# Optimization experiments

Measured on AMD Instinct MI355X. Metric: run time of the kernel, lower is better.

## Reference

```python
import jax, jax.numpy as jnp
import numpy as np

THRESH = 0.5
MARGIN = 0.1
SCALE_POS = 2.0
SCALE_NEG = 40.0
EPSILON = 1e-5


def setup_inputs() -> dict:
    key = jax.random.key(0)
    k1, k2, k3 = jax.random.split(key, 3)
    B, D = 8192, 1024
    feats = jax.random.normal(k1, (B, D), dtype=jnp.float32)
    labels = jax.random.randint(k2, (B,), 0, 128, dtype=jnp.int64)
    score = jax.random.normal(k3, (B, 3), dtype=jnp.float32)
    return {"feats": feats, "labels": labels, "score": score, "type_idx": 1}


def reference(feats, labels, score, type_idx):
    B = feats.shape[0]
    # L2 normalize (torch F.normalize eps=1e-12)
    norm = jnp.maximum(jnp.linalg.norm(feats, axis=1, keepdims=True), 1e-12)
    f = feats / norm
    sim = f @ f.T  # [B, B]

    tmp = jnp.argmax(score, axis=-1) == type_idx          # [B] selected samples
    eq = labels[:, None] == labels[None, :]               # same-label
    pair = tmp[:, None] & tmp[None, :]                    # both selected

    mask_pos_all = pair & eq                              # includes diagonal, like torch mask[i]
    count = jnp.sum(mask_pos_all, axis=1)                 # torch: sum(mask[i])
    pos0 = mask_pos_all & (sim < 1.0 - EPSILON)           # pos_pair_ after <1-eps filter
    neg0 = pair & (~eq)                                   # neg_pair_

    min_pos = jnp.min(jnp.where(pos0, sim, jnp.inf), axis=1)   # min(pos_pair_)
    max_neg = jnp.max(jnp.where(neg0, sim, -jnp.inf), axis=1)  # max(neg_pair_)

    neg_sel = neg0 & (sim + MARGIN > min_pos[:, None])    # hard negatives
    pos_sel = pos0 & (sim - MARGIN < max_neg[:, None])    # hard positives

    valid = (tmp & (count > 1)
             & jnp.any(pos0, axis=1) & jnp.any(neg0, axis=1)
             & jnp.any(neg_sel, axis=1) & jnp.any(pos_sel, axis=1))

    pos_sum = jnp.sum(jnp.where(pos_sel, jnp.exp(-SCALE_POS * (sim - THRESH)), 0.0), axis=1)
    neg_sum = jnp.sum(jnp.where(neg_sel, jnp.exp(SCALE_NEG * (sim - THRESH)), 0.0), axis=1)
    row_loss = jnp.log1p(pos_sum) / SCALE_POS + jnp.log1p(neg_sum) / SCALE_NEG

    return jnp.sum(jnp.where(valid, row_loss, 0.0)) / B
```

## Files before the change

kernel.cpp:

```cpp
#include <hip/hip_runtime.h>
#include <hip/hip_bf16.h>

typedef __attribute__((ext_vector_type(8))) short bf16x8;
typedef __attribute__((ext_vector_type(4))) float f32x4;


#define OFF_META    0
#define OFF_IDXSEL  (64*1024)
#define OFF_LBLSEL  (96*1024)
#define OFF_RLOSS   (160*1024)
#define OFF_FSEL    (256*1024)

__device__ inline unsigned short f2bf(float f){
    union { __hip_bfloat16 h; unsigned short u; } cv;
    cv.h = __float2bfloat16(f);
    return cv.u;
}

__global__ __launch_bounds__(256) void select_kernel(
    const float* __restrict__ score, const int* __restrict__ type_idx,
    const void* __restrict__ labels_raw,
    int* __restrict__ idx_sel, int* __restrict__ labels_sel,
    int* meta, int B)
{
    int tid = threadIdx.x, lane = tid & 63, wid = tid >> 6;
    int row = blockIdx.x * 256 + tid;
    __shared__ int s_is64, s_wcnt[4], s_base;

    if (wid == 0) {
        int hi = ((const int*)labels_raw)[2 * lane + 1];
        unsigned long long nz = __ballot(hi != 0);
        if (lane == 0) s_is64 = (nz == 0ULL) ? 1 : 0;
    }

    int f = 0;
    if (row < B) {
        float s0 = score[3*row], s1 = score[3*row+1], s2 = score[3*row+2];
        int am = 0; float b = s0;
        if (s1 > b) { b = s1; am = 1; }
        if (s2 > b) { am = 2; }
        f = (am == type_idx[0]) ? 1 : 0;
    }
    unsigned long long m = __ballot(f != 0);
    int incl = __popcll(m & ((2ULL << lane) - 1ULL));
    if (lane == 0) s_wcnt[wid] = __popcll(m);
    __syncthreads();
    if (tid == 0)
        s_base = atomicAdd(&meta[0], s_wcnt[0] + s_wcnt[1] + s_wcnt[2] + s_wcnt[3]);
    __syncthreads();
    if (f) {
        int prefix = 0;
        for (int w = 0; w < wid; w++) prefix += s_wcnt[w];
        int pos = s_base + prefix + incl - 1;
        idx_sel[pos] = row;
        labels_sel[pos] = s_is64 ? (int)((const long long*)labels_raw)[row]
                                 : ((const int*)labels_raw)[row];
    }
}

__global__ __launch_bounds__(256) void gather_kernel(
    const float* __restrict__ feats, const int* __restrict__ idx_sel,
    const int* __restrict__ meta, unsigned short* __restrict__ fsel, int D)
{
    int S = meta[0];
    int Spad = (S + 127) & ~127;
    int s = blockIdx.x * 4 + (threadIdx.x >> 6);
    if (s >= Spad) return;
    int lane = threadIdx.x & 63;
    ushort4* dst = (ushort4*)(fsel + (size_t)s * D);

    if (s >= S) {
        ushort4 z = {0,0,0,0};
        for (int i = lane; i < (D >> 2); i += 64) dst[i] = z;
        return;
    }

    int r = idx_sel[s];
    const float4* src = (const float4*)(feats + (size_t)r * D);

    if (D == 1024) {
        float4 v[4];
#pragma unroll
        for (int i = 0; i < 4; i++) v[i] = src[lane + i * 64];
        float ssq = 0.f;
#pragma unroll
        for (int i = 0; i < 4; i++)
            ssq += v[i].x*v[i].x + v[i].y*v[i].y + v[i].z*v[i].z + v[i].w*v[i].w;
        for (int o = 32; o; o >>= 1) ssq += __shfl_down(ssq, o);
        ssq = __shfl(ssq, 0);
        float sc = 1.0f / fmaxf(sqrtf(ssq), 1e-12f);
#pragma unroll
        for (int i = 0; i < 4; i++) {
            ushort4 o;
            o.x = f2bf(v[i].x * sc); o.y = f2bf(v[i].y * sc);
            o.z = f2bf(v[i].z * sc); o.w = f2bf(v[i].w * sc);
            dst[lane + i * 64] = o;
        }
    } else {
        int nv = D >> 2;
        float ssq = 0.f;
        for (int i = lane; i < nv; i += 64) {
            float4 v = src[i];
            ssq += v.x*v.x + v.y*v.y + v.z*v.z + v.w*v.w;
        }
        for (int o = 32; o; o >>= 1) ssq += __shfl_down(ssq, o);
        ssq = __shfl(ssq, 0);
        float sc = 1.0f / fmaxf(sqrtf(ssq), 1e-12f);
        for (int i = lane; i < nv; i += 64) {
            float4 v = src[i];
            ushort4 o;
            o.x = f2bf(v.x * sc); o.y = f2bf(v.y * sc);
            o.z = f2bf(v.z * sc); o.w = f2bf(v.w * sc);
            dst[i] = o;
        }
    }
}

__global__ __launch_bounds__(512) void simgemm_kernel(
    const unsigned short* __restrict__ fsel, const int* __restrict__ meta,
    float* __restrict__ sim, int D)
{
    int S = meta[0];
    int Spad = (S + 127) & ~127;
    int bm = blockIdx.x * 128, bn = blockIdx.y * 128;
    if (bm >= Spad || bn >= Spad) return;

    __shared__ unsigned short lA[2][1024 * 8];
    __shared__ unsigned short lB[2][1024 * 8];

    int tid = threadIdx.x;
    int lane = tid & 63;
    int wave = tid >> 6;
    int wr = (wave >> 2) * 64;
    int wc = (wave & 3) * 32;
    int laneRow = lane & 15;
    int laneK = lane >> 4;

    f32x4 acc[4][2];
#pragma unroll
    for (int m = 0; m < 4; m++)
#pragma unroll
        for (int n = 0; n < 2; n++)
            acc[m][n] = (f32x4){0.f, 0.f, 0.f, 0.f};

#define STAGE(buf, k0)                                                        \
    _Pragma("unroll")                                                         \
    for (int p = 0; p < 2; p++) {                                             \
        int c = tid + p * 512;                                                \
        int r = c >> 3, slot = c & 7;                                         \
        int og = slot ^ (r & 7);                                              \
        __builtin_amdgcn_global_load_lds(                                     \
            (const __attribute__((address_space(1))) unsigned int*)           \
                (fsel + (size_t)(bm + r) * D + (k0) + og * 8),                \
            (__attribute__((address_space(3))) unsigned int*)&lA[buf][c * 8], \
            16, 0, 0);                                                        \
        __builtin_amdgcn_global_load_lds(                                     \
            (const __attribute__((address_space(1))) unsigned int*)           \
                (fsel + (size_t)(bn + r) * D + (k0) + og * 8),                \
            (__attribute__((address_space(3))) unsigned int*)&lB[buf][c * 8], \
            16, 0, 0);                                                        \
    }

    int nt = D >> 6;
    STAGE(0, 0)
    int cur = 0;
    for (int t = 0; t < nt; t++) {
        if (t + 1 < nt) {
            STAGE(cur ^ 1, (t + 1) << 6)
            asm volatile("s_waitcnt vmcnt(4)" ::: "memory");
        } else {
            asm volatile("s_waitcnt vmcnt(0)" ::: "memory");
        }
        __builtin_amdgcn_s_barrier();
        __builtin_amdgcn_sched_barrier(0);

        bf16x8 af[2][4], bfr[2][2];
#pragma unroll
        for (int s2 = 0; s2 < 2; s2++) {
            int o = s2 * 4 + laneK;
#pragma unroll
            for (int m = 0; m < 4; m++) {
                int row = wr + m * 16 + laneRow;
                af[s2][m] = *(const bf16x8*)&lA[cur][(row * 8 + (o ^ (row & 7))) * 8];
            }
#pragma unroll
            for (int n = 0; n < 2; n++) {
                int row = wc + n * 16 + laneRow;
                bfr[s2][n] = *(const bf16x8*)&lB[cur][(row * 8 + (o ^ (row & 7))) * 8];
            }
        }
#pragma unroll
        for (int s2 = 0; s2 < 2; s2++)
#pragma unroll
            for (int m = 0; m < 4; m++)
#pragma unroll
                for (int n = 0; n < 2; n++)
                    acc[m][n] = __builtin_amdgcn_mfma_f32_16x16x32_bf16(
                        af[s2][m], bfr[s2][n], acc[m][n], 0, 0, 0);

        __builtin_amdgcn_sched_barrier(0);
        __builtin_amdgcn_s_barrier();
        cur ^= 1;
    }
#undef STAGE

#pragma unroll
    for (int m = 0; m < 4; m++) {
        int row0 = bm + wr + m * 16 + (lane >> 4) * 4;
#pragma unroll
        for (int n = 0; n < 2; n++) {
            int col = bn + wc + n * 16 + laneRow;
#pragma unroll
            for (int q = 0; q < 4; q++)
                sim[(size_t)(row0 + q) * Spad + col] = acc[m][n][q];
        }
    }
}

__global__ __launch_bounds__(256) void loss_kernel(
    const float* __restrict__ sim, const int* __restrict__ labels_sel,
    const int* __restrict__ meta, float* __restrict__ row_loss)
{
    int S = meta[0];
    if (blockIdx.x * 4 >= S) return;
    int Spad = (S + 127) & ~127;
    int tid = threadIdx.x;
    __shared__ unsigned char slbl[8192];
    for (int j = tid; j < Spad; j += 256)
        slbl[j] = (j < S) ? (unsigned char)labels_sel[j] : 0xFF;
    __syncthreads();

    int lane = tid & 63;
    int s = blockIdx.x * 4 + (tid >> 6);
    if (s >= S) return;

    const float4* rowv = (const float4*)(sim + (size_t)s * Spad);
    const unsigned* lblv = (const unsigned*)slbl;
    const float ONE_ME = 1.0f - 1e-5f;
    int lbl = slbl[s];
    int nv = Spad >> 2;

    int cnt = 0;
    float minp = INFINITY, maxn = -INFINITY;
    for (int j4 = lane; j4 < nv; j4 += 64) {
        float4 v = rowv[j4];
        unsigned lw = lblv[j4];
#pragma unroll
        for (int e = 0; e < 4; e++) {
            int j = (j4 << 2) + e;
            float sv = (&v.x)[e];
            if (j == s) sv = 1.0f;
            int lb = (lw >> (8 * e)) & 0xFF;
            if (lb == lbl) {
                cnt++;
                if (sv < ONE_ME) minp = fminf(minp, sv);
            } else if (lb != 0xFF) {
                maxn = fmaxf(maxn, sv);
            }
        }
    }
    for (int o = 32; o; o >>= 1) {
        cnt += __shfl_down(cnt, o);
        minp = fminf(minp, __shfl_down(minp, o));
        maxn = fmaxf(maxn, __shfl_down(maxn, o));
    }
    cnt  = __shfl(cnt, 0);
    minp = __shfl(minp, 0);
    maxn = __shfl(maxn, 0);

    float rl = 0.f;
    if (cnt > 1 && minp < 3e38f && maxn > -3e38f) {
        float psum = 0.f, nsum = 0.f;
        for (int j4 = lane; j4 < nv; j4 += 64) {
            float4 v = rowv[j4];
            unsigned lw = lblv[j4];
#pragma unroll
            for (int e = 0; e < 4; e++) {
                int j = (j4 << 2) + e;
                float sv = (&v.x)[e];
                if (j == s) sv = 1.0f;
                int lb = (lw >> (8 * e)) & 0xFF;
                if (lb == lbl) {
                    if (sv < ONE_ME && sv - 0.1f < maxn)
                        psum += __expf(-2.0f * (sv - 0.5f));
                } else if (lb != 0xFF) {
                    if (sv + 0.1f > minp)
                        nsum += __expf(40.0f * (sv - 0.5f));
                }
            }
        }
        for (int o = 32; o; o >>= 1) {
            psum += __shfl_down(psum, o);
            nsum += __shfl_down(nsum, o);
        }
        if (psum > 0.f && nsum > 0.f)
            rl = log1pf(psum) * 0.5f + log1pf(nsum) * 0.025f;
    }
    if (lane == 0) row_loss[s] = rl;
}

__global__ __launch_bounds__(256) void reduce_kernel(
    const float* __restrict__ row_loss, const int* __restrict__ meta,
    float* out, float invB)
{
    int S = meta[0];
    float sum = 0.f;
    for (int j = threadIdx.x; j < S; j += 256) sum += row_loss[j];
    for (int o = 32; o; o >>= 1) sum += __shfl_down(sum, o);
    __shared__ float sm[4];
    if ((threadIdx.x & 63) == 0) sm[threadIdx.x >> 6] = sum;
    __syncthreads();
    if (threadIdx.x == 0) out[0] = (sm[0] + sm[1] + sm[2] + sm[3]) * invB;
}

extern "C" void kernel_launch(void* const* d_in, const int* in_sizes, int n_in,
                              void* d_out, int out_size, void* d_ws, size_t ws_size,
                              hipStream_t stream)
{
    const float* feats    = (const float*)d_in[0];
    const void*  labels   = d_in[1];
    const float* score    = (const float*)d_in[2];
    const int*   type_idx = (const int*)d_in[3];

    int B = in_sizes[1];
    int D = in_sizes[0] / B;

    char* ws = (char*)d_ws;
    int*   meta       = (int*)  (ws + OFF_META);
    int*   idx_sel    = (int*)  (ws + OFF_IDXSEL);
    int*   labels_sel = (int*)  (ws + OFF_LBLSEL);
    float* row_loss   = (float*)(ws + OFF_RLOSS);
    unsigned short* fsel = (unsigned short*)(ws + OFF_FSEL);
    float* sim        = (float*)(ws + OFF_FSEL + (size_t)B * D * 2);
    float* out        = (float*)d_out;

    (void)hipMemsetAsync(meta, 0, 16, stream);

    select_kernel<<<(B + 255) / 256, 256, 0, stream>>>(score, type_idx, labels,
                                                       idx_sel, labels_sel, meta, B);
    gather_kernel<<<B / 4, 256, 0, stream>>>(feats, idx_sel, meta, fsel, D);
    dim3 g(B / 128, B / 128);
    simgemm_kernel<<<g, 512, 0, stream>>>(fsel, meta, sim, D);
    loss_kernel<<<B / 4, 256, 0, stream>>>(sim, labels_sel, meta, row_loss);
    reduce_kernel<<<1, 256, 0, stream>>>(row_loss, meta, out, 1.0f / (float)B);
}
```

Baseline: 138.8 us.

## Exploit sim symmetry in GEMM and register-cache rows in loss kernel

The similarity GEMM now computes only upper-triangular 128x128 tiles and writes each off-diagonal tile a second time, transposed, using f32x4 column stores, which roughly halves the MFMA work. The loss kernel, when the padded row fits in 704 float4s, keeps the whole row and its labels in registers so the second pass does not re-read global memory. The transposed stores are strided and uncoalesced, which may offset part of the GEMM savings, and the register arrays raise VGPR pressure.

Result: no change. 140.4 us (+1.2%).

```diff
diff --git a/kernel.cpp b/kernel.cpp
--- a/kernel.cpp
+++ b/kernel.cpp
@@ -124,6 +124,7 @@
     int Spad = (S + 127) & ~127;
     int bm = blockIdx.x * 128, bn = blockIdx.y * 128;
     if (bm >= Spad || bn >= Spad) return;
+    if (bm > bn) return;
 
     __shared__ unsigned short lA[2][1024 * 8];
     __shared__ unsigned short lB[2][1024 * 8];
@@ -213,6 +214,9 @@
 #pragma unroll
             for (int q = 0; q < 4; q++)
                 sim[(size_t)(row0 + q) * Spad + col] = acc[m][n][q];
+            if (bm != bn) {
+                *(f32x4*)&sim[(size_t)col * Spad + row0] = acc[m][n];
+            }
         }
     }
 }
@@ -239,62 +243,126 @@
     const float ONE_ME = 1.0f - 1e-5f;
     int lbl = slbl[s];
     int nv = Spad >> 2;
-
-    int cnt = 0;
-    float minp = INFINITY, maxn = -INFINITY;
-    for (int j4 = lane; j4 < nv; j4 += 64) {
-        float4 v = rowv[j4];
-        unsigned lw = lblv[j4];
-#pragma unroll
-        for (int e = 0; e < 4; e++) {
-            int j = (j4 << 2) + e;
-            float sv = (&v.x)[e];
-            if (j == s) sv = 1.0f;
-            int lb = (lw >> (8 * e)) & 0xFF;
-            if (lb == lbl) {
-                cnt++;
-                if (sv < ONE_ME) minp = fminf(minp, sv);
-            } else if (lb != 0xFF) {
-                maxn = fmaxf(maxn, sv);
-            }
-        }
-    }
-    for (int o = 32; o; o >>= 1) {
-        cnt += __shfl_down(cnt, o);
-        minp = fminf(minp, __shfl_down(minp, o));
-        maxn = fmaxf(maxn, __shfl_down(maxn, o));
-    }
-    cnt  = __shfl(cnt, 0);
-    minp = __shfl(minp, 0);
-    maxn = __shfl(maxn, 0);
-
     float rl = 0.f;
-    if (cnt > 1 && minp < 3e38f && maxn > -3e38f) {
-        float psum = 0.f, nsum = 0.f;
+
+    if (nv <= 704) {
+        float4 rv[11];
+        unsigned lw[11];
+#pragma unroll
+        for (int i = 0; i < 11; i++) {
+            int j4 = lane + i * 64;
+            if (j4 < nv) { rv[i] = rowv[j4]; lw[i] = lblv[j4]; }
+            else         { rv[i] = (float4){0,0,0,0}; lw[i] = 0xFFFFFFFFu; }
+        }
+        int cnt = 0;
+        float minp = INFINITY, maxn = -INFINITY;
+#pragma unroll
+        for (int i = 0; i < 11; i++) {
+            int j0 = (lane + i * 64) << 2;
+#pragma unroll
+            for (int e = 0; e < 4; e++) {
+                float sv = (&rv[i].x)[e];
+                if (j0 + e == s) sv = 1.0f;
+                int lb = (lw[i] >> (8 * e)) & 0xFF;
+                if (lb == lbl) {
+                    cnt++;
+                    if (sv < ONE_ME) minp = fminf(minp, sv);
+                } else if (lb != 0xFF) {
+                    maxn = fmaxf(maxn, sv);
+                }
+            }
+        }
+        for (int o = 32; o; o >>= 1) {
+            cnt += __shfl_down(cnt, o);
+            minp = fminf(minp, __shfl_down(minp, o));
+            maxn = fmaxf(maxn, __shfl_down(maxn, o));
+        }
+        cnt  = __shfl(cnt, 0);
+        minp = __shfl(minp, 0);
+        maxn = __shfl(maxn, 0);
+
+        if (cnt > 1 && minp < 3e38f && maxn > -3e38f) {
+            float psum = 0.f, nsum = 0.f;
+#pragma unroll
+            for (int i = 0; i < 11; i++) {
+                int j0 = (lane + i * 64) << 2;
+#pragma unroll
+                for (int e = 0; e < 4; e++) {
+                    float sv = (&rv[i].x)[e];
+                    if (j0 + e == s) sv = 1.0f;
+                    int lb = (lw[i] >> (8 * e)) & 0xFF;
+                    if (lb == lbl) {
+                        if (sv < ONE_ME && sv - 0.1f < maxn)
+                            psum += __expf(-2.0f * (sv - 0.5f));
+                    } else if (lb != 0xFF) {
+                        if (sv + 0.1f > minp)
+                            nsum += __expf(40.0f * (sv - 0.5f));
+                    }
+                }
+            }
+            for (int o = 32; o; o >>= 1) {
+                psum += __shfl_down(psum, o);
+                nsum += __shfl_down(nsum, o);
+            }
+            if (psum > 0.f && nsum > 0.f)
+                rl = log1pf(psum) * 0.5f + log1pf(nsum) * 0.025f;
+        }
+    } else {
+        int cnt = 0;
+        float minp = INFINITY, maxn = -INFINITY;
         for (int j4 = lane; j4 < nv; j4 += 64) {
             float4 v = rowv[j4];
-            unsigned lw = lblv[j4];
+            unsigned w = lblv[j4];
 #pragma unroll
             for (int e = 0; e < 4; e++) {
                 int j = (j4 << 2) + e;
                 float sv = (&v.x)[e];
                 if (j == s) sv = 1.0f;
-                int lb = (lw >> (8 * e)) & 0xFF;
+                int lb = (w >> (8 * e)) & 0xFF;
                 if (lb == lbl) {
-                    if (sv < ONE_ME && sv - 0.1f < maxn)
-                        psum += __expf(-2.0f * (sv - 0.5f));
+                    cnt++;
+                    if (sv < ONE_ME) minp = fminf(minp, sv);
                 } else if (lb != 0xFF) {
-                    if (sv + 0.1f > minp)
-                        nsum += __expf(40.0f * (sv - 0.5f));
+                    maxn = fmaxf(maxn, sv);
                 }
             }
         }
         for (int o = 32; o; o >>= 1) {
-            psum += __shfl_down(psum, o);
-            nsum += __shfl_down(nsum, o);
-        }
-        if (psum > 0.f && nsum > 0.f)
-            rl = log1pf(psum) * 0.5f + log1pf(nsum) * 0.025f;
+            cnt += __shfl_down(cnt, o);
+            minp = fminf(minp, __shfl_down(minp, o));
+            maxn = fmaxf(maxn, __shfl_down(maxn, o));
+        }
+        cnt  = __shfl(cnt, 0);
+        minp = __shfl(minp, 0);
+        maxn = __shfl(maxn, 0);
+
+        if (cnt > 1 && minp < 3e38f && maxn > -3e38f) {
+            float psum = 0.f, nsum = 0.f;
+            for (int j4 = lane; j4 < nv; j4 += 64) {
+                float4 v = rowv[j4];
+                unsigned w = lblv[j4];
+#pragma unroll
+                for (int e = 0; e < 4; e++) {
+                    int j = (j4 << 2) + e;
+                    float sv = (&v.x)[e];
+                    if (j == s) sv = 1.0f;
+                    int lb = (w >> (8 * e)) & 0xFF;
+                    if (lb == lbl) {
+                        if (sv < ONE_ME && sv - 0.1f < maxn)
+                            psum += __expf(-2.0f * (sv - 0.5f));
+                    } else if (lb != 0xFF) {
+                        if (sv + 0.1f > minp)
+                            nsum += __expf(40.0f * (sv - 0.5f));
+                    }
+                }
+            }
+            for (int o = 32; o; o >>= 1) {
+                psum += __shfl_down(psum, o);
+                nsum += __shfl_down(nsum, o);
+            }
+            if (psum > 0.f && nsum > 0.f)
+                rl = log1pf(psum) * 0.5f + log1pf(nsum) * 0.025f;
+        }
     }
     if (lane == 0) row_loss[s] = rl;
 }
```
